# Kernel tuning notes

Measured on AMD Instinct MI355X. Metric: run time of the kernel, lower is better.

Reference implementation:

```python
import jax, jax.numpy as jnp
import numpy as np

D, HIDDEN, C, N = 512, 256, 256, 8192

def setup_inputs() -> dict:
    key = jax.random.key(0)
    ks = jax.random.split(key, 12)
    s = lambda fan_in: 1.0 / np.sqrt(fan_in)
    return {
        "x":  jax.random.normal(ks[0], (N, D), dtype=jnp.float32),
        "W1": jax.random.uniform(ks[1], (D, HIDDEN), jnp.float32, -s(D), s(D)),
        "b1": jax.random.uniform(ks[2], (HIDDEN,), jnp.float32, -s(D), s(D)),
        "Wq": jax.random.uniform(ks[3], (HIDDEN, HIDDEN), jnp.float32, -s(HIDDEN), s(HIDDEN)),
        "bq": jax.random.uniform(ks[4], (HIDDEN,), jnp.float32, -s(HIDDEN), s(HIDDEN)),
        "Wk": jax.random.uniform(ks[5], (HIDDEN, HIDDEN), jnp.float32, -s(HIDDEN), s(HIDDEN)),
        "bk": jax.random.uniform(ks[6], (HIDDEN,), jnp.float32, -s(HIDDEN), s(HIDDEN)),
        "Wv": jax.random.uniform(ks[7], (HIDDEN, HIDDEN), jnp.float32, -s(HIDDEN), s(HIDDEN)),
        "bv": jax.random.uniform(ks[8], (HIDDEN,), jnp.float32, -s(HIDDEN), s(HIDDEN)),
        "a":  jax.random.uniform(ks[9], (1,), jnp.float32, 0.0, 1.0),
        "W2": jax.random.uniform(ks[10], (HIDDEN, C), jnp.float32, -s(HIDDEN), s(HIDDEN)),
        "b2": jax.random.uniform(ks[11], (C,), jnp.float32, -s(HIDDEN), s(HIDDEN)),
    }

def reference(x, W1, b1, Wq, bq, Wk, bk, Wv, bv, a, W2, b2):
    h = x @ W1 + b1                              # [N, hidden]
    q = h @ Wq + bq
    k = h @ Wk + bk
    v = h @ Wv + bv
    w = (q @ k.T) / jnp.sqrt(jnp.float32(HIDDEN))  # [N, N]
    attn = jax.nn.softmax(w, axis=0)             # non-standard: softmax over rows (dim=0)
    h = a * h + (1.0 - a) * (attn @ v)           # gated residual
    return h @ W2 + b2                           # [N, C]
```

## Files before the change

### kernel.cpp

```cpp
#include <hip/hip_runtime.h>

#define NROW 8192
#define DIM  512
#define HID  256

typedef __bf16 bf16x8 __attribute__((ext_vector_type(8)));
typedef float  f32x4  __attribute__((ext_vector_type(4)));
typedef float  f32x16 __attribute__((ext_vector_type(16)));
typedef unsigned short u16;
typedef unsigned int   u32;
typedef unsigned long long u64;
typedef u32 u32x4 __attribute__((ext_vector_type(4)));
typedef u16 u16x8 __attribute__((ext_vector_type(8)));

__device__ __forceinline__ u16 f2bf(float f) {
    u32 u = __builtin_bit_cast(u32, f);
    u32 r = (u + 0x7FFFu + ((u >> 16) & 1u)) >> 16;
    return (u16)r;
}
__device__ __forceinline__ float bf2f(u16 b) {
    u32 u = (u32)b << 16;
    return __builtin_bit_cast(float, u);
}
__device__ __forceinline__ bf16x8 ld8(const u16* p) {
    return *reinterpret_cast<const bf16x8*>(p);
}
__device__ __forceinline__ bf16x8 ld8v(const u16* p) {
    return *reinterpret_cast<const volatile bf16x8*>(p);
}
__device__ __forceinline__ void gl_lds(const u16* g, u16* l) {
    __builtin_amdgcn_global_load_lds(
        (const __attribute__((address_space(1))) void*)g,
        (__attribute__((address_space(3))) void*)l, 16, 0, 0);
}


__global__ void cvt_f32_bf16(const float* __restrict__ src, u16* __restrict__ dst, int n) {
    int idx = (blockIdx.x * blockDim.x + threadIdx.x) * 4;
    if (idx < n) {
        float4 v = *reinterpret_cast<const float4*>(src + idx);
        u64 pk = (u64)f2bf(v.x) | ((u64)f2bf(v.y) << 16) |
                 ((u64)f2bf(v.z) << 32) | ((u64)f2bf(v.w) << 48);
        *reinterpret_cast<u64*>(dst + idx) = pk;
    }
}

__global__ void cvt_wt_all(const float* __restrict__ W1, const float* __restrict__ Wq,
                           const float* __restrict__ Wk, const float* __restrict__ Wv,
                           const float* __restrict__ W2,
                           u16* __restrict__ W1T, u16* __restrict__ WqT,
                           u16* __restrict__ WkT, u16* __restrict__ WvT,
                           u16* __restrict__ W2T)
{
    int idx = blockIdx.x * 256 + threadIdx.x;
    if (idx < DIM * HID) {
        int k = idx >> 8, n = idx & 255;
        W1T[n * DIM + k] = f2bf(W1[idx]);
    } else {
        int idx2 = idx - DIM * HID;
        int sel = idx2 >> 16;
        int r   = idx2 & 65535;
        int k = r >> 8, n = r & 255;
        const float* src = sel == 0 ? Wq : sel == 1 ? Wk : sel == 2 ? Wv : W2;
        u16* dst         = sel == 0 ? WqT : sel == 1 ? WkT : sel == 2 ? WvT : W2T;
        dst[n * HID + k] = f2bf(src[r]);
    }
}

__global__ __launch_bounds__(256) void gemm_bf16(
    const u16* __restrict__ A, const u16* __restrict__ BT, const float* __restrict__ bias,
    int M, int K, int N, int mode, float scale,
    float* __restrict__ of32, u16* __restrict__ obf)
{
    const int lane  = threadIdx.x & 63;
    const int w     = threadIdx.x >> 6;
    const int row16 = lane & 15;
    const int g     = lane >> 4;
    const int i0    = blockIdx.x * 64 + w * 16;
    const int n0    = blockIdx.y * 64;

    f32x4 acc[4] = {};
    const u16* ap = A  + (size_t)(i0 + row16) * K + g * 8;
    const u16* bp = BT + (size_t)(n0 + row16) * K + g * 8;

    for (int k0 = 0; k0 < K; k0 += 32) {
        bf16x8 a = ld8(ap + k0);
#pragma unroll
        for (int nt = 0; nt < 4; ++nt) {
            bf16x8 b = ld8(bp + (size_t)nt * 16 * K + k0);
            acc[nt] = __builtin_amdgcn_mfma_f32_16x16x32_bf16(a, b, acc[nt], 0, 0, 0);
        }
    }

#pragma unroll
    for (int nt = 0; nt < 4; ++nt) {
        int col  = n0 + nt * 16 + row16;
        float bs = bias ? bias[col] : 0.0f;
        float vals[4];
#pragma unroll
        for (int r = 0; r < 4; ++r) vals[r] = (acc[nt][r] + bs) * scale;
        int rowb = i0 + g * 4;
        if (mode == 0 || mode == 1) {
#pragma unroll
            for (int r = 0; r < 4; ++r)
                of32[(size_t)(rowb + r) * N + col] = vals[r];
        }
        if (mode == 1) {
#pragma unroll
            for (int r = 0; r < 4; ++r)
                obf[(size_t)(rowb + r) * N + col] = f2bf(vals[r]);
        }
    }
}

__global__ __launch_bounds__(256) void qkv_gemm(
    const u16* __restrict__ A, const u16* __restrict__ WT,
    const float* __restrict__ bq, const float* __restrict__ bk, const float* __restrict__ bv,
    u16* __restrict__ qbf, u16* __restrict__ kbf, u16* __restrict__ vtbf)
{
    const int lane  = threadIdx.x & 63;
    const int w     = threadIdx.x >> 6;
    const int row16 = lane & 15;
    const int g     = lane >> 4;
    const int i0    = blockIdx.x * 64 + w * 16;
    const int sec   = blockIdx.y >> 2;
    const int n0l   = (blockIdx.y & 3) * 64;

    f32x4 acc[4] = {};
    const u16* ap = A  + (size_t)(i0 + row16) * HID + g * 8;
    const u16* bp = WT + (size_t)(sec * 256 + n0l + row16) * HID + g * 8;

    for (int k0 = 0; k0 < HID; k0 += 32) {
        bf16x8 a = ld8(ap + k0);
#pragma unroll
        for (int nt = 0; nt < 4; ++nt) {
            bf16x8 b = ld8(bp + (size_t)nt * 16 * HID + k0);
            acc[nt] = __builtin_amdgcn_mfma_f32_16x16x32_bf16(a, b, acc[nt], 0, 0, 0);
        }
    }

    const float* bias = sec == 0 ? bq : sec == 1 ? bk : bv;
    const float scale = sec == 0 ? 0.0625f : 1.0f;
#pragma unroll
    for (int nt = 0; nt < 4; ++nt) {
        int col  = n0l + nt * 16 + row16;
        float bs = bias[col];
        float vals[4];
#pragma unroll
        for (int r = 0; r < 4; ++r) vals[r] = (acc[nt][r] + bs) * scale;
        int rowb = i0 + g * 4;
        if (sec == 0) {
#pragma unroll
            for (int r = 0; r < 4; ++r)
                qbf[(size_t)(rowb + r) * HID + col] = f2bf(vals[r]);
        } else if (sec == 1) {
#pragma unroll
            for (int r = 0; r < 4; ++r)
                kbf[(size_t)(rowb + r) * HID + col] = f2bf(vals[r]);
        } else {
            u64 pk = (u64)f2bf(vals[0]) | ((u64)f2bf(vals[1]) << 16) |
                     ((u64)f2bf(vals[2]) << 32) | ((u64)f2bf(vals[3]) << 48);
            *reinterpret_cast<u64*>(vtbf + (size_t)col * NROW + rowb) = pk;
        }
    }
}

__global__ __launch_bounds__(256, 2) void pass_a3(
    const u16* __restrict__ qbf, const u16* __restrict__ kbf, float* __restrict__ spart)
{
    __shared__ __align__(16) u16 qlds[2][32 * 256];
    const int tid  = threadIdx.x;
    const int lane = tid & 63;
    const int w    = tid >> 6;
    const int l31  = lane & 31;
    const int g2   = lane >> 5;
    const int j0   = blockIdx.x * 128 + w * 32;
    const int ib   = blockIdx.y * (NROW / 16);
    const int nsteps = NROW / 16 / 32;

    bf16x8 kreg[16];
    {
        const u16* kp = kbf + (size_t)(j0 + l31) * HID + g2 * 8;
#pragma unroll
        for (int ks = 0; ks < 16; ++ks) kreg[ks] = ld8v(kp + ks * 16);
    }

#pragma unroll
    for (int s = 0; s < 4; ++s) {
        int c = tid + 256 * s;
        int row = c >> 5;
        gl_lds(qbf + (size_t)(ib + row) * HID + (size_t)(((c & 31) ^ row) & 31) * 8,
               &qlds[0][c * 8]);
    }

    float s_lane = 0.0f;
    for (int t = 0; t < nsteps; ++t) {
        if (t + 1 < nsteps) {
            const int r0 = ib + (t + 1) * 32;
            u16* qd = qlds[(t + 1) & 1];
#pragma unroll
            for (int s = 0; s < 4; ++s) {
                int c = tid + 256 * s;
                int row = c >> 5;
                gl_lds(qbf + (size_t)(r0 + row) * HID + (size_t)(((c & 31) ^ row) & 31) * 8,
                       qd + c * 8);
            }
            asm volatile("s_waitcnt vmcnt(4)" ::: "memory");
        } else {
            asm volatile("s_waitcnt vmcnt(0)" ::: "memory");
        }
        __builtin_amdgcn_s_barrier();
        __builtin_amdgcn_sched_barrier(0);

        const u16* qb = qlds[t & 1];
        f32x16 s0 = {}, s1 = {};
#pragma unroll
        for (int ks = 0; ks < 8; ++ks) {
            bf16x8 qf0 = *reinterpret_cast<const bf16x8*>(
                &qb[l31 * 256 + (((ks * 2 + g2) ^ l31) & 31) * 8]);
            s0 = __builtin_amdgcn_mfma_f32_32x32x16_bf16(qf0, kreg[ks], s0, 0, 0, 0);
            bf16x8 qf1 = *reinterpret_cast<const bf16x8*>(
                &qb[l31 * 256 + ((((ks + 8) * 2 + g2) ^ l31) & 31) * 8]);
            s1 = __builtin_amdgcn_mfma_f32_32x32x16_bf16(qf1, kreg[ks + 8], s1, 0, 0, 0);
        }
#pragma unroll
        for (int r = 0; r < 16; ++r) s_lane += __expf(s0[r] + s1[r]);
        __builtin_amdgcn_s_barrier();
    }
    s_lane += __shfl_xor(s_lane, 32);
    if (lane < 32) spart[(size_t)blockIdx.y * NROW + j0 + l31] = s_lane;
}

__global__ void merge_stats2(const float* __restrict__ spart, float* __restrict__ sinv) {
    int j = blockIdx.x * 256 + threadIdx.x;
    float s = 0.0f;
#pragma unroll
    for (int p = 0; p < 16; ++p) s += spart[(size_t)p * NROW + j];
    sinv[j] = 1.0f / s;
}

__global__ void scale_vt(u16* __restrict__ vt, const float* __restrict__ sinv) {
    int idx = (blockIdx.x * 256 + threadIdx.x) * 8;
    int j = idx & (NROW - 1);
    u16x8 v = *reinterpret_cast<const u16x8*>(&vt[idx]);
    float4 s0 = *reinterpret_cast<const float4*>(&sinv[j]);
    float4 s1 = *reinterpret_cast<const float4*>(&sinv[j + 4]);
    float sc[8] = {s0.x, s0.y, s0.z, s0.w, s1.x, s1.y, s1.z, s1.w};
    u16x8 o;
#pragma unroll
    for (int e = 0; e < 8; ++e) o[e] = f2bf(bf2f(v[e]) * sc[e]);
    *reinterpret_cast<u16x8*>(&vt[idx]) = o;
}

__global__ __launch_bounds__(256, 1) void pass_b2(
    const u16* __restrict__ qbf, const u16* __restrict__ kbf, const u16* __restrict__ vtbf,
    u16* __restrict__ pvp, int NS)
{
    __shared__ __align__(16) u16 kbuf[2][64 * 256];
    __shared__ __align__(16) u16 vbuf[2][128 * 128];
    const int tid  = threadIdx.x;
    const int lane = tid & 63;
    const int w    = tid >> 6;
    const int l31  = lane & 31;
    const int g2   = lane >> 5;
    const int i0   = blockIdx.x * 128 + w * 32;
    const int jn   = NROW / NS;
    const int jb   = blockIdx.y * jn;
    const int nsteps = jn / 64;

    bf16x8 qreg[16];
    {
        const u16* qp = qbf + (size_t)(i0 + l31) * HID + g2 * 8;
#pragma unroll
        for (int ks = 0; ks < 16; ++ks) qreg[ks] = ld8v(qp + ks * 16);
    }
    f32x16 acc[8] = {};

    {
        const int j0 = jb;
#pragma unroll
        for (int s = 0; s < 8; ++s) {
            int c = tid + 256 * s;
            int row = c >> 5;
            gl_lds(kbf + (size_t)(j0 + row) * HID + (size_t)(((c & 31) ^ row) & 31) * 8,
                   &kbuf[0][c * 8]);
        }
#pragma unroll
        for (int s = 0; s < 8; ++s) {
            int c = tid + 256 * s;
            int row = c >> 4, sl = (c & 15) ^ (row & 15);
            int d = row * 2 + (sl >> 3);
            gl_lds(vtbf + (size_t)d * NROW + j0 + (sl & 7) * 8, &vbuf[0][c * 8]);
        }
        asm volatile("s_waitcnt vmcnt(0)" ::: "memory");
        __builtin_amdgcn_s_barrier();
    }

    for (int t = 0; t < nsteps; ++t) {
        const int cur = t & 1;
        const u16* kb = kbuf[cur];
        const u16* vb = vbuf[cur];
        if (t + 1 < nsteps) {
            const int j0 = jb + (t + 1) * 64;
            u16* kd = kbuf[cur ^ 1];
            u16* vd = vbuf[cur ^ 1];
#pragma unroll
            for (int s = 0; s < 8; ++s) {
                int c = tid + 256 * s;
                int row = c >> 5;
                gl_lds(kbf + (size_t)(j0 + row) * HID + (size_t)(((c & 31) ^ row) & 31) * 8,
                       kd + c * 8);
            }
#pragma unroll
            for (int s = 0; s < 8; ++s) {
                int c = tid + 256 * s;
                int row = c >> 4, sl = (c & 15) ^ (row & 15);
                int d = row * 2 + (sl >> 3);
                gl_lds(vtbf + (size_t)d * NROW + j0 + (sl & 7) * 8, vd + c * 8);
            }
            asm volatile("s_waitcnt vmcnt(16)" ::: "memory");
        } else {
            asm volatile("s_waitcnt vmcnt(0)" ::: "memory");
        }
        __builtin_amdgcn_s_barrier();

#pragma unroll
        for (int jj = 0; jj < 2; ++jj) {
            f32x16 sacc = {};
#pragma unroll
            for (int ks = 0; ks < 16; ++ks) {
                int row = jj * 32 + l31;
                bf16x8 kf = *reinterpret_cast<const bf16x8*>(
                    &kb[row * 256 + (((ks * 2 + g2) ^ l31) & 31) * 8]);
                sacc = __builtin_amdgcn_mfma_f32_32x32x16_bf16(kf, qreg[ks], sacc, 0, 0, 0);
            }
            float p[16];
#pragma unroll
            for (int r = 0; r < 16; ++r) p[r] = __expf(sacc[r]);
            u32 q0a, q0b, q1a, q1b, q2a, q2b, q3a, q3b;
            asm("v_cvt_pk_bf16_f32 %0, %1, %2" : "=v"(q0a) : "v"(p[0]),  "v"(p[1]));
            asm("v_cvt_pk_bf16_f32 %0, %1, %2" : "=v"(q0b) : "v"(p[2]),  "v"(p[3]));
            asm("v_cvt_pk_bf16_f32 %0, %1, %2" : "=v"(q1a) : "v"(p[4]),  "v"(p[5]));
            asm("v_cvt_pk_bf16_f32 %0, %1, %2" : "=v"(q1b) : "v"(p[6]),  "v"(p[7]));
            asm("v_cvt_pk_bf16_f32 %0, %1, %2" : "=v"(q2a) : "v"(p[8]),  "v"(p[9]));
            asm("v_cvt_pk_bf16_f32 %0, %1, %2" : "=v"(q2b) : "v"(p[10]), "v"(p[11]));
            asm("v_cvt_pk_bf16_f32 %0, %1, %2" : "=v"(q3a) : "v"(p[12]), "v"(p[13]));
            asm("v_cvt_pk_bf16_f32 %0, %1, %2" : "=v"(q3b) : "v"(p[14]), "v"(p[15]));
            asm volatile("v_permlane32_swap_b32 %0, %1" : "+v"(q0a), "+v"(q1a));
            asm volatile("v_permlane32_swap_b32 %0, %1" : "+v"(q0b), "+v"(q1b));
            asm volatile("v_permlane32_swap_b32 %0, %1" : "+v"(q2a), "+v"(q3a));
            asm volatile("v_permlane32_swap_b32 %0, %1" : "+v"(q2b), "+v"(q3b));
            u32x4 f0v = {q0a, q0b, q1a, q1b};
            u32x4 f1v = {q2a, q2b, q3a, q3b};
            bf16x8 F0 = __builtin_bit_cast(bf16x8, f0v);
            bf16x8 F1 = __builtin_bit_cast(bf16x8, f1v);
#pragma unroll
            for (int m = 0; m < 2; ++m) {
                bf16x8 pf = (m == 0) ? F0 : F1;
#pragma unroll
                for (int dt = 0; dt < 8; ++dt) {
                    int row = dt * 16 + (l31 >> 1);
                    int sl = ((l31 & 1) << 3) | (jj * 4 + m * 2 + g2);
                    bf16x8 vf = *reinterpret_cast<const bf16x8*>(
                        &vb[row * 128 + ((sl ^ (row & 15)) & 15) * 8]);
                    acc[dt] = __builtin_amdgcn_mfma_f32_32x32x16_bf16(pf, vf, acc[dt], 0, 0, 0);
                }
            }
        }
        __builtin_amdgcn_s_barrier();
    }

    u16* op = pvp + (size_t)blockIdx.y * NROW * HID;
#pragma unroll
    for (int dt = 0; dt < 8; ++dt) {
#pragma unroll
        for (int r = 0; r < 16; ++r) {
            int i = i0 + (r & 3) + 8 * (r >> 2) + 4 * g2;
            op[(size_t)i * HID + dt * 32 + l31] = f2bf(acc[dt][r]);
        }
    }
}

__global__ void merge_gate2(const u16* __restrict__ pvp, const float* __restrict__ hF,
                            const float* __restrict__ a, u16* __restrict__ hgbf, int NS)
{
    int idx = (blockIdx.x * 256 + threadIdx.x) * 8;
    float av = a[0];
    float s[8] = {};
    for (int p = 0; p < NS; ++p) {
        u16x8 v = *reinterpret_cast<const u16x8*>(&pvp[(size_t)p * NROW * HID + idx]);
#pragma unroll
        for (int e = 0; e < 8; ++e) s[e] += bf2f(v[e]);
    }
    float4 h0 = *reinterpret_cast<const float4*>(&hF[idx]);
    float4 h1 = *reinterpret_cast<const float4*>(&hF[idx + 4]);
    float hv[8] = {h0.x, h0.y, h0.z, h0.w, h1.x, h1.y, h1.z, h1.w};
    u16x8 o;
#pragma unroll
    for (int e = 0; e < 8; ++e) o[e] = f2bf(av * hv[e] + (1.0f - av) * s[e]);
    *reinterpret_cast<u16x8*>(&hgbf[idx]) = o;
}


extern "C" void kernel_launch(void* const* d_in, const int* in_sizes, int n_in,
                              void* d_out, int out_size, void* d_ws, size_t ws_size,
                              hipStream_t stream)
{
    const float* x  = (const float*)d_in[0];
    const float* W1 = (const float*)d_in[1];
    const float* b1 = (const float*)d_in[2];
    const float* Wq = (const float*)d_in[3];
    const float* bq = (const float*)d_in[4];
    const float* Wk = (const float*)d_in[5];
    const float* bk = (const float*)d_in[6];
    const float* Wv = (const float*)d_in[7];
    const float* bv = (const float*)d_in[8];
    const float* a  = (const float*)d_in[9];
    const float* W2 = (const float*)d_in[10];
    const float* b2 = (const float*)d_in[11];
    float* out = (float*)d_out;

    const int NS = (ws_size >= (size_t)64 * 1024 * 1024) ? 8 : 4;

    char* ws = (char*)d_ws;
    size_t off = 0;
    auto alloc = [&](size_t bytes) {
        char* p = ws + off;
        off += (bytes + 255) & ~(size_t)255;
        return p;
    };
    u16* W1T  = (u16*)alloc((size_t)DIM * HID * 2);
    u16* WqT  = (u16*)alloc((size_t)HID * HID * 2);
    u16* WkT  = (u16*)alloc((size_t)HID * HID * 2);
    u16* WvT  = (u16*)alloc((size_t)HID * HID * 2);
    u16* W2T  = (u16*)alloc((size_t)HID * HID * 2);
    float* hF = (float*)alloc((size_t)NROW * HID * 4);
    u16* hbf  = (u16*)alloc((size_t)NROW * HID * 2);
    u16* qbf  = (u16*)alloc((size_t)NROW * HID * 2);
    u16* kbf  = (u16*)alloc((size_t)NROW * HID * 2);
    u16* vtbf = (u16*)alloc((size_t)HID * NROW * 2);
    float* spart = (float*)alloc((size_t)16 * NROW * 4);
    float* sinv  = (float*)alloc((size_t)NROW * 4);
    u16* hgbf = (u16*)alloc((size_t)NROW * HID * 2);
    char* un = alloc((size_t)NS * NROW * HID * 2 > (size_t)NROW * DIM * 2
                         ? (size_t)NS * NROW * HID * 2 : (size_t)NROW * DIM * 2);
    u16* xbf = (u16*)un;
    u16* pvp = (u16*)un;
    (void)in_sizes; (void)n_in; (void)out_size;

    cvt_f32_bf16<<<NROW * DIM / (256 * 4), 256, 0, stream>>>(x, xbf, NROW * DIM);
    cvt_wt_all<<<(DIM * HID + 4 * HID * HID) / 256, 256, 0, stream>>>(
        W1, Wq, Wk, Wv, W2, W1T, WqT, WkT, WvT, W2T);

    gemm_bf16<<<dim3(NROW / 64, HID / 64), 256, 0, stream>>>(
        xbf, W1T, b1, NROW, DIM, HID, 1, 1.0f, hF, hbf);
    qkv_gemm<<<dim3(NROW / 64, 12), 256, 0, stream>>>(
        hbf, WqT, bq, bk, bv, qbf, kbf, vtbf);

    pass_a3<<<dim3(NROW / 128, 16), 256, 0, stream>>>(qbf, kbf, spart);
    merge_stats2<<<NROW / 256, 256, 0, stream>>>(spart, sinv);
    scale_vt<<<HID * NROW / (256 * 8), 256, 0, stream>>>(vtbf, sinv);
    pass_b2<<<dim3(NROW / 128, NS), 256, 0, stream>>>(qbf, kbf, vtbf, pvp, NS);
    merge_gate2<<<NROW * HID / (256 * 8), 256, 0, stream>>>(pvp, hF, a, hgbf, NS);

    gemm_bf16<<<dim3(NROW / 64, HID / 64), 256, 0, stream>>>(
        hgbf, W2T, b2, NROW, HID, HID, 0, 1.0f, out, nullptr);
}
```

Measured before the change: 314.4 us.

## Halve pass_b tile depth for two blocks per CU and interleave split-K blocks

The attention P·V pass now streams K/V tiles of 32 keys instead of 64. This halves the double-buffered LDS footprint so that launch bounds can allow two blocks per CU. The QK^T reduction is split into two independent accumulators to expose MFMA ILP, and s_setprio is raised around the MFMA sections. The grid is flattened so that the split-K index varies fastest, which places blocks sharing K/V slices far apart. The workspace layout is also changed so hbf aliases the pvp scratch, letting the 8-way split fit in a smaller workspace. The costs are more barriers per key and register pressure under the 2-block occupancy limit.

```diff
diff --git a/kernel.cpp b/kernel.cpp
--- a/kernel.cpp
+++ b/kernel.cpp
@@ -252,21 +252,24 @@
     *reinterpret_cast<u16x8*>(&vt[idx]) = o;
 }
 
-__global__ __launch_bounds__(256, 1) void pass_b2(
+__global__ __launch_bounds__(256, 2) void pass_b3(
     const u16* __restrict__ qbf, const u16* __restrict__ kbf, const u16* __restrict__ vtbf,
-    u16* __restrict__ pvp, int NS)
-{
-    __shared__ __align__(16) u16 kbuf[2][64 * 256];
-    __shared__ __align__(16) u16 vbuf[2][128 * 128];
+    u16* __restrict__ pvp, int NS, int ns_shift)
+{
+    __shared__ __align__(16) u16 kbuf[2][32 * 256];
+    __shared__ __align__(16) u16 vbuf[2][64 * 128];
     const int tid  = threadIdx.x;
     const int lane = tid & 63;
     const int w    = tid >> 6;
     const int l31  = lane & 31;
     const int g2   = lane >> 5;
-    const int i0   = blockIdx.x * 128 + w * 32;
+    const int bid  = blockIdx.x;
+    const int ys   = bid & (NS - 1);
+    const int xs   = bid >> ns_shift;
+    const int i0   = xs * 128 + w * 32;
     const int jn   = NROW / NS;
-    const int jb   = blockIdx.y * jn;
-    const int nsteps = jn / 64;
+    const int jb   = ys * jn;
+    const int nsteps = jn / 32;
 
     bf16x8 qreg[16];
     {
@@ -276,101 +279,101 @@
     }
     f32x16 acc[8] = {};
 
-    {
-        const int j0 = jb;
-#pragma unroll
-        for (int s = 0; s < 8; ++s) {
-            int c = tid + 256 * s;
-            int row = c >> 5;
-            gl_lds(kbf + (size_t)(j0 + row) * HID + (size_t)(((c & 31) ^ row) & 31) * 8,
-                   &kbuf[0][c * 8]);
-        }
-#pragma unroll
-        for (int s = 0; s < 8; ++s) {
-            int c = tid + 256 * s;
-            int row = c >> 4, sl = (c & 15) ^ (row & 15);
-            int d = row * 2 + (sl >> 3);
-            gl_lds(vtbf + (size_t)d * NROW + j0 + (sl & 7) * 8, &vbuf[0][c * 8]);
-        }
-        asm volatile("s_waitcnt vmcnt(0)" ::: "memory");
-        __builtin_amdgcn_s_barrier();
+#pragma unroll
+    for (int s = 0; s < 4; ++s) {
+        int c = tid + 256 * s;
+        int row = c >> 5, sl = c & 31;
+        gl_lds(kbf + (size_t)(jb + row) * HID + (size_t)((sl ^ row) & 31) * 8,
+               &kbuf[0][c * 8]);
+    }
+#pragma unroll
+    for (int s = 0; s < 4; ++s) {
+        int c = tid + 256 * s;
+        int row = c >> 4, sl = (c & 15) ^ (row & 15);
+        int d = row * 4 + (sl >> 2);
+        gl_lds(vtbf + (size_t)d * NROW + jb + (sl & 3) * 8, &vbuf[0][c * 8]);
     }
 
     for (int t = 0; t < nsteps; ++t) {
         const int cur = t & 1;
+        if (t + 1 < nsteps) {
+            const int j0 = jb + (t + 1) * 32;
+            u16* kd = kbuf[cur ^ 1];
+            u16* vd = vbuf[cur ^ 1];
+#pragma unroll
+            for (int s = 0; s < 4; ++s) {
+                int c = tid + 256 * s;
+                int row = c >> 5, sl = c & 31;
+                gl_lds(kbf + (size_t)(j0 + row) * HID + (size_t)((sl ^ row) & 31) * 8,
+                       kd + c * 8);
+            }
+#pragma unroll
+            for (int s = 0; s < 4; ++s) {
+                int c = tid + 256 * s;
+                int row = c >> 4, sl = (c & 15) ^ (row & 15);
+                int d = row * 4 + (sl >> 2);
+                gl_lds(vtbf + (size_t)d * NROW + j0 + (sl & 3) * 8, vd + c * 8);
+            }
+            asm volatile("s_waitcnt vmcnt(8)" ::: "memory");
+        } else {
+            asm volatile("s_waitcnt vmcnt(0)" ::: "memory");
+        }
+        __builtin_amdgcn_s_barrier();
+
         const u16* kb = kbuf[cur];
         const u16* vb = vbuf[cur];
-        if (t + 1 < nsteps) {
-            const int j0 = jb + (t + 1) * 64;
-            u16* kd = kbuf[cur ^ 1];
-            u16* vd = vbuf[cur ^ 1];
-#pragma unroll
-            for (int s = 0; s < 8; ++s) {
-                int c = tid + 256 * s;
-                int row = c >> 5;
-                gl_lds(kbf + (size_t)(j0 + row) * HID + (size_t)(((c & 31) ^ row) & 31) * 8,
-                       kd + c * 8);
+
+        f32x16 s0 = {}, s1 = {};
+        __builtin_amdgcn_s_setprio(1);
+#pragma unroll
+        for (int ks = 0; ks < 8; ++ks) {
+            bf16x8 kf0 = *reinterpret_cast<const bf16x8*>(
+                &kb[l31 * 256 + (((ks * 2 + g2) ^ l31) & 31) * 8]);
+            s0 = __builtin_amdgcn_mfma_f32_32x32x16_bf16(kf0, qreg[ks], s0, 0, 0, 0);
+            bf16x8 kf1 = *reinterpret_cast<const bf16x8*>(
+                &kb[l31 * 256 + ((((ks + 8) * 2 + g2) ^ l31) & 31) * 8]);
+            s1 = __builtin_amdgcn_mfma_f32_32x32x16_bf16(kf1, qreg[ks + 8], s1, 0, 0, 0);
+        }
+        __builtin_amdgcn_s_setprio(0);
+
+        float p[16];
+#pragma unroll
+        for (int r = 0; r < 16; ++r) p[r] = __expf(s0[r] + s1[r]);
+        u32 q0a, q0b, q1a, q1b, q2a, q2b, q3a, q3b;
+        asm("v_cvt_pk_bf16_f32 %0, %1, %2" : "=v"(q0a) : "v"(p[0]),  "v"(p[1]));
+        asm("v_cvt_pk_bf16_f32 %0, %1, %2" : "=v"(q0b) : "v"(p[2]),  "v"(p[3]));
+        asm("v_cvt_pk_bf16_f32 %0, %1, %2" : "=v"(q1a) : "v"(p[4]),  "v"(p[5]));
+        asm("v_cvt_pk_bf16_f32 %0, %1, %2" : "=v"(q1b) : "v"(p[6]),  "v"(p[7]));
+        asm("v_cvt_pk_bf16_f32 %0, %1, %2" : "=v"(q2a) : "v"(p[8]),  "v"(p[9]));
+        asm("v_cvt_pk_bf16_f32 %0, %1, %2" : "=v"(q2b) : "v"(p[10]), "v"(p[11]));
+        asm("v_cvt_pk_bf16_f32 %0, %1, %2" : "=v"(q3a) : "v"(p[12]), "v"(p[13]));
+        asm("v_cvt_pk_bf16_f32 %0, %1, %2" : "=v"(q3b) : "v"(p[14]), "v"(p[15]));
+        asm volatile("v_permlane32_swap_b32 %0, %1" : "+v"(q0a), "+v"(q1a));
+        asm volatile("v_permlane32_swap_b32 %0, %1" : "+v"(q0b), "+v"(q1b));
+        asm volatile("v_permlane32_swap_b32 %0, %1" : "+v"(q2a), "+v"(q3a));
+        asm volatile("v_permlane32_swap_b32 %0, %1" : "+v"(q2b), "+v"(q3b));
+        u32x4 f0v = {q0a, q0b, q1a, q1b};
+        u32x4 f1v = {q2a, q2b, q3a, q3b};
+        bf16x8 F0 = __builtin_bit_cast(bf16x8, f0v);
+        bf16x8 F1 = __builtin_bit_cast(bf16x8, f1v);
+
+        __builtin_amdgcn_s_setprio(1);
+#pragma unroll
+        for (int m = 0; m < 2; ++m) {
+            bf16x8 pf = (m == 0) ? F0 : F1;
+#pragma unroll
+            for (int dt = 0; dt < 8; ++dt) {
+                int row = dt * 8 + (l31 >> 2);
+                int sl = ((((l31 & 3) << 2) | (m * 2 + g2)) ^ (row & 15)) & 15;
+                bf16x8 vf = *reinterpret_cast<const bf16x8*>(&vb[row * 128 + sl * 8]);
+                acc[dt] = __builtin_amdgcn_mfma_f32_32x32x16_bf16(pf, vf, acc[dt], 0, 0, 0);
             }
-#pragma unroll
-            for (int s = 0; s < 8; ++s) {
-                int c = tid + 256 * s;
-                int row = c >> 4, sl = (c & 15) ^ (row & 15);
-                int d = row * 2 + (sl >> 3);
-                gl_lds(vtbf + (size_t)d * NROW + j0 + (sl & 7) * 8, vd + c * 8);
-            }
-            asm volatile("s_waitcnt vmcnt(16)" ::: "memory");
-        } else {
-            asm volatile("s_waitcnt vmcnt(0)" ::: "memory");
-        }
+        }
+        __builtin_amdgcn_s_setprio(0);
         __builtin_amdgcn_s_barrier();
-
-#pragma unroll
-        for (int jj = 0; jj < 2; ++jj) {
-            f32x16 sacc = {};
-#pragma unroll
-            for (int ks = 0; ks < 16; ++ks) {
-                int row = jj * 32 + l31;
-                bf16x8 kf = *reinterpret_cast<const bf16x8*>(
-                    &kb[row * 256 + (((ks * 2 + g2) ^ l31) & 31) * 8]);
-                sacc = __builtin_amdgcn_mfma_f32_32x32x16_bf16(kf, qreg[ks], sacc, 0, 0, 0);
-            }
-            float p[16];
-#pragma unroll
-            for (int r = 0; r < 16; ++r) p[r] = __expf(sacc[r]);
-            u32 q0a, q0b, q1a, q1b, q2a, q2b, q3a, q3b;
-            asm("v_cvt_pk_bf16_f32 %0, %1, %2" : "=v"(q0a) : "v"(p[0]),  "v"(p[1]));
-            asm("v_cvt_pk_bf16_f32 %0, %1, %2" : "=v"(q0b) : "v"(p[2]),  "v"(p[3]));
-            asm("v_cvt_pk_bf16_f32 %0, %1, %2" : "=v"(q1a) : "v"(p[4]),  "v"(p[5]));
-            asm("v_cvt_pk_bf16_f32 %0, %1, %2" : "=v"(q1b) : "v"(p[6]),  "v"(p[7]));
-            asm("v_cvt_pk_bf16_f32 %0, %1, %2" : "=v"(q2a) : "v"(p[8]),  "v"(p[9]));
-            asm("v_cvt_pk_bf16_f32 %0, %1, %2" : "=v"(q2b) : "v"(p[10]), "v"(p[11]));
-            asm("v_cvt_pk_bf16_f32 %0, %1, %2" : "=v"(q3a) : "v"(p[12]), "v"(p[13]));
-            asm("v_cvt_pk_bf16_f32 %0, %1, %2" : "=v"(q3b) : "v"(p[14]), "v"(p[15]));
-            asm volatile("v_permlane32_swap_b32 %0, %1" : "+v"(q0a), "+v"(q1a));
-            asm volatile("v_permlane32_swap_b32 %0, %1" : "+v"(q0b), "+v"(q1b));
-            asm volatile("v_permlane32_swap_b32 %0, %1" : "+v"(q2a), "+v"(q3a));
-            asm volatile("v_permlane32_swap_b32 %0, %1" : "+v"(q2b), "+v"(q3b));
-            u32x4 f0v = {q0a, q0b, q1a, q1b};
-            u32x4 f1v = {q2a, q2b, q3a, q3b};
-            bf16x8 F0 = __builtin_bit_cast(bf16x8, f0v);
-            bf16x8 F1 = __builtin_bit_cast(bf16x8, f1v);
-#pragma unroll
-            for (int m = 0; m < 2; ++m) {
-                bf16x8 pf = (m == 0) ? F0 : F1;
-#pragma unroll
-                for (int dt = 0; dt < 8; ++dt) {
-                    int row = dt * 16 + (l31 >> 1);
-                    int sl = ((l31 & 1) << 3) | (jj * 4 + m * 2 + g2);
-                    bf16x8 vf = *reinterpret_cast<const bf16x8*>(
-                        &vb[row * 128 + ((sl ^ (row & 15)) & 15) * 8]);
-                    acc[dt] = __builtin_amdgcn_mfma_f32_32x32x16_bf16(pf, vf, acc[dt], 0, 0, 0);
-                }
-            }
-        }
-        __builtin_amdgcn_s_barrier();
-    }
-
-    u16* op = pvp + (size_t)blockIdx.y * NROW * HID;
+    }
+
+    u16* op = pvp + (size_t)ys * NROW * HID;
 #pragma unroll
     for (int dt = 0; dt < 8; ++dt) {
 #pragma unroll
@@ -420,7 +423,8 @@
     const float* b2 = (const float*)d_in[11];
     float* out = (float*)d_out;
 
-    const int NS = (ws_size >= (size_t)64 * 1024 * 1024) ? 8 : 4;
+    const int NS = (ws_size >= (size_t)60 * 1024 * 1024) ? 8 : 4;
+    const int ns_shift = (NS == 8) ? 3 : 2;
 
     char* ws = (char*)d_ws;
     size_t off = 0;
@@ -435,16 +439,17 @@
     u16* WvT  = (u16*)alloc((size_t)HID * HID * 2);
     u16* W2T  = (u16*)alloc((size_t)HID * HID * 2);
     float* hF = (float*)alloc((size_t)NROW * HID * 4);
-    u16* hbf  = (u16*)alloc((size_t)NROW * HID * 2);
     u16* qbf  = (u16*)alloc((size_t)NROW * HID * 2);
     u16* kbf  = (u16*)alloc((size_t)NROW * HID * 2);
     u16* vtbf = (u16*)alloc((size_t)HID * NROW * 2);
     float* spart = (float*)alloc((size_t)16 * NROW * 4);
     float* sinv  = (float*)alloc((size_t)NROW * 4);
     u16* hgbf = (u16*)alloc((size_t)NROW * HID * 2);
-    char* un = alloc((size_t)NS * NROW * HID * 2 > (size_t)NROW * DIM * 2
-                         ? (size_t)NS * NROW * HID * 2 : (size_t)NROW * DIM * 2);
+    size_t xh = (size_t)NROW * DIM * 2 + (size_t)NROW * HID * 2;
+    size_t pv = (size_t)NS * NROW * HID * 2;
+    char* un = alloc(pv > xh ? pv : xh);
     u16* xbf = (u16*)un;
+    u16* hbf = (u16*)(un + (size_t)NROW * DIM * 2);
     u16* pvp = (u16*)un;
     (void)in_sizes; (void)n_in; (void)out_size;
 
@@ -460,7 +465,7 @@
     pass_a3<<<dim3(NROW / 128, 16), 256, 0, stream>>>(qbf, kbf, spart);
     merge_stats2<<<NROW / 256, 256, 0, stream>>>(spart, sinv);
     scale_vt<<<HID * NROW / (256 * 8), 256, 0, stream>>>(vtbf, sinv);
-    pass_b2<<<dim3(NROW / 128, NS), 256, 0, stream>>>(qbf, kbf, vtbf, pvp, NS);
+    pass_b3<<<64 * NS, 256, 0, stream>>>(qbf, kbf, vtbf, pvp, NS, ns_shift);
     merge_gate2<<<NROW * HID / (256 * 8), 256, 0, stream>>>(pvp, hF, a, hgbf, NS);
 
     gemm_bf16<<<dim3(NROW / 64, HID / 64), 256, 0, stream>>>(
```

Result: slower. 352.9 us (+12.2%).
